# Optimization experiments

Hardware: AMD Instinct MI355X
Metric: run time of the kernel (lower is better)

The kernel has to match this reference:

```python
import jax, jax.numpy as jnp
import numpy as np

B, S, D, H, P = 4, 4096, 1024, 8, 32
K = D // H  # head_dim = 128


def setup_inputs() -> dict:
    key = jax.random.key(0)
    ks = jax.random.split(key, 12)
    f = lambda k, shape, s: jax.random.normal(k, shape, dtype=jnp.float32) * s
    return {
        "x": f(ks[0], (B, S, D), 1.0),
        "W_proj": f(ks[1], (H, K, D), 0.03),
        "resonance_freqs": f(ks[2], (H, K), 0.01),
        "pol_W": f(ks[3], (H, P, K), 0.08),
        "pol_b": jnp.zeros((H, P), jnp.float32),
        "imp_W1": f(ks[4], (16, 1), 0.5),               # Linear(1, 16)
        "imp_b1": jnp.zeros((16,), jnp.float32),
        "imp_W2": f(ks[5], (1, 16), 0.25),              # Linear(16, 1)
        "imp_b2": jnp.zeros((1,), jnp.float32),
        "out_W": f(ks[6], (D, D), 0.03),                # Linear(dim, dim)
        "out_b": jnp.zeros((D,), jnp.float32),
        "ln_g": jnp.ones((D,), jnp.float32),
        "ln_b": jnp.zeros((D,), jnp.float32),
        "causal": 1,
    }


def reference(x, W_proj, resonance_freqs, pol_W, pol_b, imp_W1, imp_b1,
              imp_W2, imp_b2, out_W, out_b, ln_g, ln_b, causal):
    Bx, Sx, Dx = x.shape
    nH = W_proj.shape[0]
    # per-head projection + resonance frequency modulation -> (B, H, S, K)
    heads = jnp.einsum('bsd,hkd->bhsk', x, W_proj)
    heads = heads * jnp.cos(resonance_freqs * jnp.pi)[None, :, None, :]

    # --- GuaXiangDuiChong: learned cross-head impedance ---
    summary = heads.mean(axis=2)                                   # (B, H, K)
    pol = jnp.tanh(jnp.einsum('bhk,hpk->bhp', summary, pol_W) + pol_b[None])
    pol = pol / jnp.maximum(jnp.linalg.norm(pol, axis=-1, keepdims=True), 1e-12)
    dots = jnp.einsum('bhp,bgp->bhg', pol, pol)                    # (B, H, H)
    z = dots[..., None]                                            # (B, H, H, 1)
    hid = jax.nn.gelu(z * imp_W1[:, 0] + imp_b1, approximate=False)  # (B, H, H, 16)
    imp = jax.nn.softplus(jnp.einsum('bijc,oc->bijo', hid, imp_W2) + imp_b2)[..., 0]
    eye = jnp.eye(nH, dtype=x.dtype)
    impedance = imp * (1.0 - eye)                                  # (B, H, H)

    # --- cross-head transfer ---
    # h_i += sum_{j != i} heads_j / (1 + imp[i,j]) * 0.1, causally mean-masked.
    coef = (0.1 / (1.0 + impedance)) * (1.0 - eye)                 # zero diagonal (i == j skipped)
    transfer = jnp.einsum('bij,bjsk->bisk', coef, heads)           # (B, H, S, K)
    if causal and Sx > 1:
        # masked_fill(t>s)+mean over t of a key-independent tensor == scale by (s+1)/S
        scale = (jnp.arange(Sx, dtype=x.dtype) + 1.0) / Sx
        transfer = transfer * scale[None, None, :, None]
    out_heads = heads + transfer

    merged = out_heads.transpose(0, 2, 1, 3).reshape(Bx, Sx, Dx)   # cat heads on last dim
    y = merged @ out_W.T + out_b + x                               # dropout is identity in eval
    mu = y.mean(-1, keepdims=True)
    var = ((y - mu) ** 2).mean(-1, keepdims=True)
    normed = (y - mu) / jnp.sqrt(var + 1e-5) * ln_g + ln_b
    return normed, impedance
```

## Files before the change

### kernel.cpp

```cpp
#include <hip/hip_runtime.h>

typedef __bf16 bf16x8 __attribute__((ext_vector_type(8)));
typedef float f32x4 __attribute__((ext_vector_type(4)));
typedef unsigned short us8 __attribute__((ext_vector_type(8)));

#define PI_F 3.14159265358979323846f

__device__ __forceinline__ unsigned short f2bf(float f) {
    unsigned u = __float_as_uint(f);
    u += 0x7FFFu + ((u >> 16) & 1u);
    return (unsigned short)(u >> 16);
}
__device__ __forceinline__ float bf2f(unsigned short h) {
    return __uint_as_float(((unsigned)h) << 16);
}

__device__ __forceinline__ void async16(const void* g, void* l) {
    __builtin_amdgcn_global_load_lds(
        (const __attribute__((address_space(1))) unsigned int*)g,
        (__attribute__((address_space(3))) unsigned int*)l, 16, 0, 0);
}

__global__ __launch_bounds__(256) void prep_k(const float* __restrict__ W,
                                              const float* __restrict__ fr,
                                              const float* __restrict__ Wo,
                                              unsigned short* __restrict__ W1b,
                                              unsigned short* __restrict__ Wob) {
    int idx = blockIdx.x * 256 + threadIdx.x;
    if (idx < (1 << 20)) {
        int n = idx >> 10, d = idx & 1023;
        int k = n >> 3, h = n & 7;
        float c = cosf(fr[h * 128 + k] * PI_F);
        W1b[idx] = f2bf(W[((h * 128 + k) << 10) + d] * c);
    } else {
        int i2 = idx - (1 << 20);
        int n = i2 >> 10, dp = i2 & 1023;
        int k = dp >> 3, h = dp & 7;
        Wob[i2] = f2bf(Wo[(n << 10) + h * 128 + k]);
    }
}

__global__ __launch_bounds__(256) void xbar_cast(const float* __restrict__ x,
                                                 unsigned short* __restrict__ xb,
                                                 float* __restrict__ part) {
    int bid = blockIdx.x;
    int b = bid >> 8;
    int s0 = (bid & 255) * 16;
    int t = threadIdx.x;
    float a0 = 0.f, a1 = 0.f, a2 = 0.f, a3 = 0.f;
    for (int i = 0; i < 16; ++i) {
        long row = (long)b * 4096 + s0 + i;
        float4 v = ((const float4*)x)[row * 256 + t];
        a0 += v.x; a1 += v.y; a2 += v.z; a3 += v.w;
        ushort4 u;
        u.x = f2bf(v.x); u.y = f2bf(v.y); u.z = f2bf(v.z); u.w = f2bf(v.w);
        ((ushort4*)xb)[row * 256 + t] = u;
    }
    float4 p; p.x = a0; p.y = a1; p.z = a2; p.w = a3;
    ((float4*)part)[bid * 256 + t] = p;
}

__global__ __launch_bounds__(256) void xbar_r(const float* __restrict__ part,
                                              float* __restrict__ xbar) {
    __shared__ float sl[256];
    int blk = blockIdx.x;
    int b = blk >> 3, dgrp = blk & 7;
    int t = threadIdx.x;
    int col = dgrp * 128 + (t & 127);
    int ih = t >> 7;
    float s = 0.f;
    for (int i = 0; i < 128; ++i) {
        int cb = b * 256 + ih * 128 + i;
        s += part[cb * 1024 + col];
    }
    sl[t] = s;
    __syncthreads();
    if (t < 128) xbar[b * 1024 + col] = sl[t] + sl[t + 128];
}

__global__ __launch_bounds__(256) void summary_k(const float* __restrict__ xbar,
                                                 const float* __restrict__ W,
                                                 const float* __restrict__ fr,
                                                 float* __restrict__ summary) {
    int wave = (blockIdx.x * 256 + threadIdx.x) >> 6;
    int lane = threadIdx.x & 63;
    int b = wave >> 10, hk = wave & 1023;
    int h = hk >> 7, k = hk & 127;
    const float* wrow = &W[(h * 128 + k) << 10];
    const float* xrow = &xbar[b << 10];
    float s = 0.f;
    for (int d = lane; d < 1024; d += 64) s += xrow[d] * wrow[d];
    for (int off = 32; off; off >>= 1) s += __shfl_down(s, off);
    if (lane == 0) {
        float c = cosf(fr[h * 128 + k] * PI_F);
        summary[wave] = s * c * (1.0f / 4096.0f);
    }
}

__global__ __launch_bounds__(256) void imp_k(const float* __restrict__ summary,
                                             const float* __restrict__ pol_W,
                                             const float* __restrict__ pol_b,
                                             const float* __restrict__ imp_W1,
                                             const float* __restrict__ imp_b1,
                                             const float* __restrict__ imp_W2,
                                             const float* __restrict__ imp_b2,
                                             float* __restrict__ coef_out,
                                             float* __restrict__ imp_out) {
    __shared__ float pol[4][8][32];
    __shared__ float rn[32];
    int t = threadIdx.x;
    for (int o = t; o < 1024; o += 256) {
        int b = o >> 8, h = (o >> 5) & 7, p = o & 31;
        const float* srow = &summary[(b * 8 + h) * 128];
        const float* wrow = &pol_W[(h * 32 + p) * 128];
        float acc = pol_b[h * 32 + p];
        for (int k = 0; k < 128; ++k) acc += srow[k] * wrow[k];
        pol[b][h][p] = tanhf(acc);
    }
    __syncthreads();
    if (t < 32) {
        int b = t >> 3, h = t & 7;
        float ss = 0.f;
        for (int p = 0; p < 32; ++p) { float v = pol[b][h][p]; ss += v * v; }
        rn[t] = 1.0f / fmaxf(sqrtf(ss), 1e-12f);
    }
    __syncthreads();
    {
        int b = t >> 6, i = (t >> 3) & 7, j = t & 7;
        float d = 0.f;
        for (int p = 0; p < 32; ++p) d += pol[b][i][p] * pol[b][j][p];
        d *= rn[b * 8 + i] * rn[b * 8 + j];
        float s = imp_b2[0];
        for (int c = 0; c < 16; ++c) {
            float z = d * imp_W1[c] + imp_b1[c];
            float gl = 0.5f * z * (1.0f + erff(z * 0.70710678118654752f));
            s += gl * imp_W2[c];
        }
        float sp = fmaxf(s, 0.0f) + log1pf(expf(-fabsf(s)));
        float impv = (i == j) ? 0.0f : sp;
        imp_out[t] = impv;
        coef_out[t] = (i == j) ? 0.0f : 0.1f / (1.0f + impv);
    }
}

__device__ __forceinline__ void swizzle_blk(int n, long& rowBase, long& colBase) {
    int xcd = n & 7, s = n >> 3;
    rowBase = (long)(xcd * 16 + (s & 15)) * 128;
    colBase = (long)(s >> 4) * 128;
}

#define GEMM_CORE(A_, B_, As_, Bs_)                                            \
    const int wave = t >> 6;                                                   \
    const int lane = t & 63;                                                   \
    const int wr = wave >> 1, wc = wave & 1;                                   \
    const int lr8 = lane >> 3;                             \
    const int gr = lane & 7;                                      \
    const int sw = ((gr ^ lr8) << 4);    \
    const char* gA = (const char*)A_ + (rowBase + wave * 32 + lr8) * 2048 + sw;\
    const char* gB = (const char*)B_ + (colBase + wave * 32 + lr8) * 2048 + sw;\
    char* lA = (char*)As_ + wave * 4096;                                       \
    char* lB = (char*)Bs_ + wave * 4096;                                       \
    const int q = lane >> 4;                                                   \
    const int c16 = lane & 15;                                                 \
    const int xorm = c16 & 7;                                                  \
    const int oA0 = ((q ^ xorm) << 4);                 \
    const int oA1 = (((4 + q) ^ xorm) << 4);           \
    const int aRow = (wr * 64 + c16) * 128;                                    \
    const int bRow = (wc * 64 + c16) * 128;                                    \
    f32x4 acc[4][4] = {};                                                      \
    for (int kt = 0; kt < 2048; kt += 128) {                                   \
        const char* a0 = gA + kt;                                              \
        const char* b0 = gB + kt;                                              \
        async16(a0, lA);                                                       \
        async16(a0 + 8 * 2048, lA + 1024);                                     \
        async16(a0 + 16 * 2048, lA + 2048);                                    \
        async16(a0 + 24 * 2048, lA + 3072);                                    \
        async16(b0, lB);                                                       \
        async16(b0 + 8 * 2048, lB + 1024);                                     \
        async16(b0 + 16 * 2048, lB + 2048);                                    \
        async16(b0 + 24 * 2048, lB + 3072);                                    \
        __syncthreads();                                                       \
        bf16x8 af[2][4], bfr[2][4];                                            \
        _Pragma("unroll")                                                      \
        for (int mi = 0; mi < 4; ++mi) {                                       \
            af[0][mi] = *(const bf16x8*)((const char*)As_ + aRow + mi * 2048 + oA0); \
            af[1][mi] = *(const bf16x8*)((const char*)As_ + aRow + mi * 2048 + oA1); \
        }                                                                      \
        _Pragma("unroll")                                                      \
        for (int ni = 0; ni < 4; ++ni) {                                       \
            bfr[0][ni] = *(const bf16x8*)((const char*)Bs_ + bRow + ni * 2048 + oA0); \
            bfr[1][ni] = *(const bf16x8*)((const char*)Bs_ + bRow + ni * 2048 + oA1); \
        }                                                                      \
        _Pragma("unroll")                                                      \
        for (int h = 0; h < 2; ++h)                                            \
            _Pragma("unroll")                                                  \
            for (int mi = 0; mi < 4; ++mi)                                     \
                _Pragma("unroll")                                              \
                for (int ni = 0; ni < 4; ++ni)                                 \
                    acc[mi][ni] = __builtin_amdgcn_mfma_f32_16x16x32_bf16(     \
                        af[h][mi], bfr[h][ni], acc[mi][ni], 0, 0, 0);          \
        __syncthreads();                                                       \
    }

__global__ __launch_bounds__(256, 3) void gemm1_mix(const unsigned short* __restrict__ A,
                                                    const unsigned short* __restrict__ B,
                                                    const float* __restrict__ coef,
                                                    const int* __restrict__ causal,
                                                    unsigned short* __restrict__ C) {
    __shared__ float mixs[64 * 132];
    __shared__ float cfs[64];
    unsigned short* As = (unsigned short*)mixs;
    unsigned short* Bs = As + 8192;
    const int t = threadIdx.x;
    long rowBase, colBase;
    swizzle_blk(blockIdx.x, rowBase, colBase);
    const int b = (int)(rowBase >> 12);
    if (t < 64) cfs[t] = coef[b * 64 + t];
    const int causalv = causal[0];

    GEMM_CORE(A, B, As, Bs)

#pragma unroll
    for (int pass = 0; pass < 2; ++pass) {
        if (wr == pass) {
#pragma unroll
            for (int mi = 0; mi < 4; ++mi)
#pragma unroll
                for (int ni = 0; ni < 4; ++ni)
#pragma unroll
                    for (int r = 0; r < 4; ++r)
                        mixs[(mi * 16 + q * 4 + r) * 132 + wc * 64 + ni * 16 + c16] = acc[mi][ni][r];
        }
        __syncthreads();
        long rb2 = rowBase + pass * 64;
#pragma unroll
        for (int it = 0; it < 4; ++it) {
            int item = t + it * 256;
            int r = item >> 4, kg = item & 15;
            const float* src = mixs + r * 132 + kg * 8;
            float v[8];
#pragma unroll
            for (int j = 0; j < 8; ++j) v[j] = src[j];
            long row = rb2 + r;
            float scale = causalv ? (float)((row & 4095) + 1) * (1.0f / 4096.0f) : 1.0f;
            us8 o;
#pragma unroll
            for (int i = 0; i < 8; ++i) {
                float ts = 0.f;
#pragma unroll
                for (int j = 0; j < 8; ++j) ts += cfs[i * 8 + j] * v[j];
                o[i] = f2bf(v[i] + scale * ts);
            }
            *(us8*)(C + row * 1024 + colBase + kg * 8) = o;
        }
        __syncthreads();
    }
}

__global__ __launch_bounds__(256, 3) void gemm_bt(const unsigned short* __restrict__ A,
                                                  const unsigned short* __restrict__ B,
                                                  unsigned short* __restrict__ C) {
    __shared__ unsigned short As[128 * 64];
    __shared__ unsigned short Bs[128 * 64];
    const int t = threadIdx.x;
    long rowBase, colBase;
    swizzle_blk(blockIdx.x, rowBase, colBase);

    GEMM_CORE(A, B, As, Bs)

#pragma unroll
    for (int mi = 0; mi < 4; ++mi) {
#pragma unroll
        for (int ni = 0; ni < 4; ++ni) {
            long col = colBase + wc * 64 + ni * 16 + c16;
            long row0 = rowBase + wr * 64 + mi * 16 + q * 4;
#pragma unroll
            for (int r = 0; r < 4; ++r)
                C[(row0 + r) * 1024 + col] = f2bf(acc[mi][ni][r]);
        }
    }
}

__global__ __launch_bounds__(256) void ln_k(const unsigned short* __restrict__ ypre,
                                            const float* __restrict__ x,
                                            const float* __restrict__ outb,
                                            const float* __restrict__ gam,
                                            const float* __restrict__ bet,
                                            float* __restrict__ out) {
    int row = blockIdx.x;
    int t = threadIdx.x;
    long base = (long)row * 1024 + t * 4;
    ushort4 yp = *(const ushort4*)(ypre + base);
    float4 xv = *(const float4*)(x + base);
    float4 bv = *(const float4*)(outb + t * 4);
    float y0 = bf2f(yp.x) + xv.x + bv.x;
    float y1 = bf2f(yp.y) + xv.y + bv.y;
    float y2 = bf2f(yp.z) + xv.z + bv.z;
    float y3 = bf2f(yp.w) + xv.w + bv.w;
    float s = y0 + y1 + y2 + y3;
    float ss = y0 * y0 + y1 * y1 + y2 * y2 + y3 * y3;
    for (int off = 32; off; off >>= 1) {
        s += __shfl_down(s, off);
        ss += __shfl_down(ss, off);
    }
    __shared__ float red[8];
    int wv = t >> 6, ln = t & 63;
    if (ln == 0) { red[wv] = s; red[4 + wv] = ss; }
    __syncthreads();
    if (t == 0) {
        float S1 = red[0] + red[1] + red[2] + red[3];
        float S2 = red[4] + red[5] + red[6] + red[7];
        float mu = S1 * (1.0f / 1024.0f);
        float var = S2 * (1.0f / 1024.0f) - mu * mu;
        red[0] = mu;
        red[1] = 1.0f / sqrtf(var + 1e-5f);
    }
    __syncthreads();
    float mu = red[0], rs = red[1];
    float4 gv = *(const float4*)(gam + t * 4);
    float4 bb = *(const float4*)(bet + t * 4);
    float4 o;
    o.x = (y0 - mu) * rs * gv.x + bb.x;
    o.y = (y1 - mu) * rs * gv.y + bb.y;
    o.z = (y2 - mu) * rs * gv.z + bb.z;
    o.w = (y3 - mu) * rs * gv.w + bb.w;
    *(float4*)(out + base) = o;
}

extern "C" void kernel_launch(void* const* d_in, const int* in_sizes, int n_in,
                              void* d_out, int out_size, void* d_ws, size_t ws_size,
                              hipStream_t stream) {
    const float* x       = (const float*)d_in[0];
    const float* W_proj  = (const float*)d_in[1];
    const float* freqs   = (const float*)d_in[2];
    const float* pol_W   = (const float*)d_in[3];
    const float* pol_b   = (const float*)d_in[4];
    const float* imp_W1  = (const float*)d_in[5];
    const float* imp_b1  = (const float*)d_in[6];
    const float* imp_W2  = (const float*)d_in[7];
    const float* imp_b2  = (const float*)d_in[8];
    const float* out_W   = (const float*)d_in[9];
    const float* out_b   = (const float*)d_in[10];
    const float* ln_g    = (const float*)d_in[11];
    const float* ln_b    = (const float*)d_in[12];
    const int*   causal  = (const int*)d_in[13];
    float* out = (float*)d_out;

    char* ws = (char*)d_ws;
    unsigned short* xb      = (unsigned short*)(ws + 0);
    unsigned short* merged  = (unsigned short*)(ws + 33554432);
    unsigned short* w1b     = (unsigned short*)(ws + 67108864);
    unsigned short* wob     = (unsigned short*)(ws + 69206016);
    float* xbar             = (float*)(ws + 71303168);
    float* summary          = (float*)(ws + 71319552);
    float* coef             = (float*)(ws + 71335936);
    float* part             = (float*)merged;
    unsigned short* ypre    = xb;

    prep_k<<<8192, 256, 0, stream>>>(W_proj, freqs, out_W, w1b, wob);
    xbar_cast<<<1024, 256, 0, stream>>>(x, xb, part);
    xbar_r<<<32, 256, 0, stream>>>(part, xbar);
    summary_k<<<1024, 256, 0, stream>>>(xbar, W_proj, freqs, summary);
    imp_k<<<1, 256, 0, stream>>>(summary, pol_W, pol_b, imp_W1, imp_b1,
                                 imp_W2, imp_b2, coef, out + 16777216);
    gemm1_mix<<<1024, 256, 0, stream>>>(xb, w1b, coef, causal, merged);
    gemm_bt<<<1024, 256, 0, stream>>>(merged, wob, ypre);
    ln_k<<<16384, 256, 0, stream>>>(ypre, x, out_b, ln_g, ln_b, out);
}
```

Measured before the change: 319.3 us.

## Halve GEMM K-tile, drop LDS swizzle, chunk mix epilogue, remove LayerNorm barrier

The shared GEMM core now stages 32-element K slices per iteration instead of 64, with two async loads per operand and no XOR swizzle on the LDS layout. LDS per block shrinks to 16 KB. The gemm1_mix epilogue is reworked to stage 16 rows at a time through the smaller buffer, in 8 passes. The LayerNorm kernel has every thread compute mean and rstd itself, which removes one barrier. The smaller LDS footprint may allow more resident blocks, but it doubles the number of K-loop barriers and may bring back LDS bank conflicts.

```diff
diff --git a/kernel.cpp b/kernel.cpp
--- a/kernel.cpp
+++ b/kernel.cpp
@@ -153,52 +153,38 @@
     const int wave = t >> 6;                                                   \
     const int lane = t & 63;                                                   \
     const int wr = wave >> 1, wc = wave & 1;                                   \
-    const int lr8 = lane >> 3;                             \
-    const int gr = lane & 7;                                      \
-    const int sw = ((gr ^ lr8) << 4);    \
-    const char* gA = (const char*)A_ + (rowBase + wave * 32 + lr8) * 2048 + sw;\
-    const char* gB = (const char*)B_ + (colBase + wave * 32 + lr8) * 2048 + sw;\
-    char* lA = (char*)As_ + wave * 4096;                                       \
-    char* lB = (char*)Bs_ + wave * 4096;                                       \
+    const int lr = lane >> 2;                                                  \
+    const int lb = (lane & 3) * 16;                                            \
+    const char* gA = (const char*)A_ + (rowBase + wave * 32 + lr) * 2048 + lb; \
+    const char* gB = (const char*)B_ + (colBase + wave * 32 + lr) * 2048 + lb; \
+    char* lA = (char*)As_ + wave * 2048;                                       \
+    char* lB = (char*)Bs_ + wave * 2048;                                       \
     const int q = lane >> 4;                                                   \
     const int c16 = lane & 15;                                                 \
-    const int xorm = c16 & 7;                                                  \
-    const int oA0 = ((q ^ xorm) << 4);                 \
-    const int oA1 = (((4 + q) ^ xorm) << 4);           \
-    const int aRow = (wr * 64 + c16) * 128;                                    \
-    const int bRow = (wc * 64 + c16) * 128;                                    \
     f32x4 acc[4][4] = {};                                                      \
-    for (int kt = 0; kt < 2048; kt += 128) {                                   \
-        const char* a0 = gA + kt;                                              \
-        const char* b0 = gB + kt;                                              \
+    for (int kt = 0; kt < 1024; kt += 32) {                                    \
+        const char* a0 = gA + kt * 2;                                          \
+        const char* b0 = gB + kt * 2;                                          \
         async16(a0, lA);                                                       \
-        async16(a0 + 8 * 2048, lA + 1024);                                     \
-        async16(a0 + 16 * 2048, lA + 2048);                                    \
-        async16(a0 + 24 * 2048, lA + 3072);                                    \
+        async16(a0 + 16 * 2048, lA + 1024);                                    \
         async16(b0, lB);                                                       \
-        async16(b0 + 8 * 2048, lB + 1024);                                     \
-        async16(b0 + 16 * 2048, lB + 2048);                                    \
-        async16(b0 + 24 * 2048, lB + 3072);                                    \
+        async16(b0 + 16 * 2048, lB + 1024);                                    \
         __syncthreads();                                                       \
-        bf16x8 af[2][4], bfr[2][4];                                            \
+        bf16x8 af[4], bfr[4];                                                  \
         _Pragma("unroll")                                                      \
-        for (int mi = 0; mi < 4; ++mi) {                                       \
-            af[0][mi] = *(const bf16x8*)((const char*)As_ + aRow + mi * 2048 + oA0); \
-            af[1][mi] = *(const bf16x8*)((const char*)As_ + aRow + mi * 2048 + oA1); \
-        }                                                                      \
+        for (int mi = 0; mi < 4; ++mi)                                         \
+            af[mi] = *(const bf16x8*)((const char*)As_ +                       \
+                       ((wr * 64 + mi * 16 + c16) * 32 + q * 8) * 2);          \
         _Pragma("unroll")                                                      \
-        for (int ni = 0; ni < 4; ++ni) {                                       \
-            bfr[0][ni] = *(const bf16x8*)((const char*)Bs_ + bRow + ni * 2048 + oA0); \
-            bfr[1][ni] = *(const bf16x8*)((const char*)Bs_ + bRow + ni * 2048 + oA1); \
-        }                                                                      \
+        for (int ni = 0; ni < 4; ++ni)                                         \
+            bfr[ni] = *(const bf16x8*)((const char*)Bs_ +                      \
+                       ((wc * 64 + ni * 16 + c16) * 32 + q * 8) * 2);          \
         _Pragma("unroll")                                                      \
-        for (int h = 0; h < 2; ++h)                                            \
+        for (int mi = 0; mi < 4; ++mi)                                         \
             _Pragma("unroll")                                                  \
-            for (int mi = 0; mi < 4; ++mi)                                     \
-                _Pragma("unroll")                                              \
-                for (int ni = 0; ni < 4; ++ni)                                 \
-                    acc[mi][ni] = __builtin_amdgcn_mfma_f32_16x16x32_bf16(     \
-                        af[h][mi], bfr[h][ni], acc[mi][ni], 0, 0, 0);          \
+            for (int ni = 0; ni < 4; ++ni)                                     \
+                acc[mi][ni] = __builtin_amdgcn_mfma_f32_16x16x32_bf16(         \
+                    af[mi], bfr[ni], acc[mi][ni], 0, 0, 0);                    \
         __syncthreads();                                                       \
     }
 
@@ -207,10 +193,11 @@
                                                     const float* __restrict__ coef,
                                                     const int* __restrict__ causal,
                                                     unsigned short* __restrict__ C) {
-    __shared__ float mixs[64 * 132];
+    __shared__ char smem[16384];
     __shared__ float cfs[64];
-    unsigned short* As = (unsigned short*)mixs;
-    unsigned short* Bs = As + 8192;
+    unsigned short* As = (unsigned short*)smem;
+    unsigned short* Bs = (unsigned short*)(smem + 8192);
+    float* mixt = (float*)smem;
     const int t = threadIdx.x;
     long rowBase, colBase;
     swizzle_blk(blockIdx.x, rowBase, colBase);
@@ -220,39 +207,33 @@
 
     GEMM_CORE(A, B, As, Bs)
 
-#pragma unroll
-    for (int pass = 0; pass < 2; ++pass) {
-        if (wr == pass) {
-#pragma unroll
-            for (int mi = 0; mi < 4; ++mi)
-#pragma unroll
-                for (int ni = 0; ni < 4; ++ni)
-#pragma unroll
-                    for (int r = 0; r < 4; ++r)
-                        mixs[(mi * 16 + q * 4 + r) * 132 + wc * 64 + ni * 16 + c16] = acc[mi][ni][r];
+    const int r16 = t >> 4, kg = t & 15;
+#pragma unroll
+    for (int p = 0; p < 8; ++p) {
+        if (wr == (p >> 2)) {
+            int mi = p & 3;
+#pragma unroll
+            for (int ni = 0; ni < 4; ++ni)
+#pragma unroll
+                for (int r = 0; r < 4; ++r)
+                    mixt[(q * 4 + r) * 132 + wc * 64 + ni * 16 + c16] = acc[mi][ni][r];
         }
         __syncthreads();
-        long rb2 = rowBase + pass * 64;
-#pragma unroll
-        for (int it = 0; it < 4; ++it) {
-            int item = t + it * 256;
-            int r = item >> 4, kg = item & 15;
-            const float* src = mixs + r * 132 + kg * 8;
-            float v[8];
-#pragma unroll
-            for (int j = 0; j < 8; ++j) v[j] = src[j];
-            long row = rb2 + r;
-            float scale = causalv ? (float)((row & 4095) + 1) * (1.0f / 4096.0f) : 1.0f;
-            us8 o;
-#pragma unroll
-            for (int i = 0; i < 8; ++i) {
-                float ts = 0.f;
-#pragma unroll
-                for (int j = 0; j < 8; ++j) ts += cfs[i * 8 + j] * v[j];
-                o[i] = f2bf(v[i] + scale * ts);
-            }
-            *(us8*)(C + row * 1024 + colBase + kg * 8) = o;
+        const float* src = mixt + r16 * 132 + kg * 8;
+        float v[8];
+#pragma unroll
+        for (int j = 0; j < 8; ++j) v[j] = src[j];
+        long row = rowBase + p * 16 + r16;
+        float scale = causalv ? (float)((row & 4095) + 1) * (1.0f / 4096.0f) : 1.0f;
+        us8 o;
+#pragma unroll
+        for (int i = 0; i < 8; ++i) {
+            float ts = 0.f;
+#pragma unroll
+            for (int j = 0; j < 8; ++j) ts += cfs[i * 8 + j] * v[j];
+            o[i] = f2bf(v[i] + scale * ts);
         }
+        *(us8*)(C + row * 1024 + colBase + kg * 8) = o;
         __syncthreads();
     }
 }
@@ -260,8 +241,8 @@
 __global__ __launch_bounds__(256, 3) void gemm_bt(const unsigned short* __restrict__ A,
                                                   const unsigned short* __restrict__ B,
                                                   unsigned short* __restrict__ C) {
-    __shared__ unsigned short As[128 * 64];
-    __shared__ unsigned short Bs[128 * 64];
+    __shared__ unsigned short As[128 * 32];
+    __shared__ unsigned short Bs[128 * 32];
     const int t = threadIdx.x;
     long rowBase, colBase;
     swizzle_blk(blockIdx.x, rowBase, colBase);
@@ -307,16 +288,11 @@
     int wv = t >> 6, ln = t & 63;
     if (ln == 0) { red[wv] = s; red[4 + wv] = ss; }
     __syncthreads();
-    if (t == 0) {
-        float S1 = red[0] + red[1] + red[2] + red[3];
-        float S2 = red[4] + red[5] + red[6] + red[7];
-        float mu = S1 * (1.0f / 1024.0f);
-        float var = S2 * (1.0f / 1024.0f) - mu * mu;
-        red[0] = mu;
-        red[1] = 1.0f / sqrtf(var + 1e-5f);
-    }
-    __syncthreads();
-    float mu = red[0], rs = red[1];
+    float S1 = red[0] + red[1] + red[2] + red[3];
+    float S2 = red[4] + red[5] + red[6] + red[7];
+    float mu = S1 * (1.0f / 1024.0f);
+    float var = S2 * (1.0f / 1024.0f) - mu * mu;
+    float rs = 1.0f / sqrtf(var + 1e-5f);
     float4 gv = *(const float4*)(gam + t * 4);
     float4 bb = *(const float4*)(bet + t * 4);
     float4 o;
```

After: 300.5 us. -5.9%, faster.
